# Kernel optimization log

Hardware: AMD Instinct MI355X
Metric: run time of the kernel (lower is better)

Reference implementation:

```python
import jax, jax.numpy as jnp
import numpy as np

B, T, H = 4, 1024, 4096
N_Q, N_KV, HD = 32, 8, 128
N_REP = N_Q // N_KV
THETA = 10000.0


def setup_inputs() -> dict:
    key = jax.random.key(0)
    k0, k1, k2 = jax.random.split(key, 3)
    x = jax.random.normal(k0, (B, T, H), dtype=jnp.float32)
    w_qkv = jax.random.normal(k1, ((N_Q + 2 * N_KV) * HD, H), dtype=jnp.float32) * 0.02
    w_proj = jax.random.normal(k2, (N_Q * HD, H), dtype=jnp.float32).T * 0.02  # [H, N_Q*HD] -> stored as [out,in]=[4096,4096]
    # real RoPE frequencies, matching precompute_freqs_cis(theta=10000)
    inv_freq = 1.0 / (THETA ** (np.arange(0, HD, 2, dtype=np.float32) / HD))  # [HD/2]
    angles = np.arange(T, dtype=np.float32)[:, None] * inv_freq[None, :]      # [T, HD/2]
    freqs_cos = jnp.asarray(np.cos(angles))
    freqs_sin = jnp.asarray(np.sin(angles))
    return {"x": x, "w_qkv": w_qkv, "w_proj": w_proj,
            "freqs_cos": freqs_cos, "freqs_sin": freqs_sin}


def _rope(x, cos, sin):
    # x: [B, T, nH, HD]; consecutive pairs (x[2i], x[2i+1]) form complex numbers
    x0 = x[..., 0::2]
    x1 = x[..., 1::2]
    c = cos[None, :, None, :]
    s = sin[None, :, None, :]
    r0 = x0 * c - x1 * s
    r1 = x0 * s + x1 * c
    return jnp.stack([r0, r1], axis=-1).reshape(x.shape)


def reference(x, w_qkv, w_proj, freqs_cos, freqs_sin):
    q_per_kv = N_Q // N_KV
    qkv = jnp.einsum('bth,oh->bto', x, w_qkv)                 # [B,T,(N_Q+2*N_KV)*HD]
    qkv = qkv.reshape(B, T, N_KV, q_per_kv + 2, HD)           # interleaved GQA layout
    q = qkv[:, :, :, :q_per_kv, :].reshape(B, T, N_Q, HD)
    k = qkv[:, :, :, q_per_kv, :]                              # [B,T,N_KV,HD]
    v = qkv[:, :, :, q_per_kv + 1, :]
    q = _rope(q, freqs_cos, freqs_sin)
    k = _rope(k, freqs_cos, freqs_sin)
    k = jnp.repeat(k, N_REP, axis=2)                           # [B,T,N_Q,HD]
    v = jnp.repeat(v, N_REP, axis=2)
    q = q.transpose(0, 2, 1, 3)                                # [B,H,T,HD]
    k = k.transpose(0, 2, 1, 3)
    v = v.transpose(0, 2, 1, 3)
    scale = 1.0 / jnp.sqrt(jnp.float32(HD))
    scores = jnp.einsum('bhqd,bhkd->bhqk', q, k) * scale       # [B,H,T,T]
    causal = jnp.tril(jnp.ones((T, T), dtype=bool))
    scores = jnp.where(causal[None, None], scores, jnp.finfo(scores.dtype).min)
    attn = jax.nn.softmax(scores, axis=-1)
    out = jnp.einsum('bhqk,bhkd->bhqd', attn, v)               # [B,H,T,HD]
    out = out.transpose(0, 2, 1, 3).reshape(B, T, N_Q * HD)
    return jnp.einsum('bto,ho->bth', out, w_proj)              # RowParallel proj, [B,T,H]
```

## Files before the change

kernel.cpp:

```cpp
#include <hip/hip_runtime.h>
#include <cstddef>

#define DEVINL __device__ __forceinline__

typedef float f32x4 __attribute__((ext_vector_type(4)));
typedef __bf16 bf16x8 __attribute__((ext_vector_type(8)));

DEVINL unsigned short f2bf(float f) {
  union { float f; unsigned int u; } v; v.f = f;
  unsigned int u = v.u;
  unsigned int r = (u + 0x7fffu + ((u >> 16) & 1u)) >> 16;
  return (unsigned short)r;
}
DEVINL float bf2f(unsigned short s) {
  union { unsigned int u; float f; } v; v.u = ((unsigned int)s) << 16;
  return v.f;
}
DEVINL uint4 pack8(const unsigned short o[8]) {
  uint4 r;
  r.x = (unsigned int)o[0] | ((unsigned int)o[1] << 16);
  r.y = (unsigned int)o[2] | ((unsigned int)o[3] << 16);
  r.z = (unsigned int)o[4] | ((unsigned int)o[5] << 16);
  r.w = (unsigned int)o[6] | ((unsigned int)o[7] << 16);
  return r;
}
DEVINL void gload16(const void* g, void* l) {
  __builtin_amdgcn_global_load_lds(
      (__attribute__((address_space(1))) void*)g,
      (__attribute__((address_space(3))) void*)l, 16, 0, 0);
}

__global__ __launch_bounds__(256) void k_cvt(const float* __restrict__ in,
                                             unsigned short* __restrict__ out, int n4) {
  int i = blockIdx.x * 256 + threadIdx.x;
  if (i >= n4) return;
  float4 v = ((const float4*)in)[i];
  ushort4 o;
  o.x = f2bf(v.x); o.y = f2bf(v.y); o.z = f2bf(v.z); o.w = f2bf(v.w);
  ((ushort4*)out)[i] = o;
}

template <int OUT_BF16>
__global__ __launch_bounds__(512, 1) void k_gemm256(const unsigned short* __restrict__ A,
                                                    const unsigned short* __restrict__ Bt,
                                                    void* __restrict__ Cout,
                                                    int M, int N, int K) {
  __shared__ __align__(16) unsigned short As[2][2][256 * 32];
  __shared__ __align__(16) unsigned short Bs[2][2][256 * 32];
  const int t = threadIdx.x, lane = t & 63;
  const int wid = t >> 6, wm = wid >> 2, wn = wid & 3;
  const int fr = lane & 15, kq = lane >> 4;
  const int nwg = gridDim.x * gridDim.y;
  int lin = blockIdx.y * gridDim.x + blockIdx.x;
  lin = (lin & 7) * (nwg >> 3) + (lin >> 3);
  const int bx = lin % gridDim.x, by = lin / gridDim.x;
  const int row0 = by * 256, col0 = bx * 256;
  const int NT = K >> 6;

  int srow[2], sgs[2];
#pragma unroll
  for (int i = 0; i < 2; ++i) {
    const int off = (i * 512 + t) * 16;
    srow[i] = off >> 6;
    sgs[i] = (((off >> 4) & 3) - (srow[i] >> 1)) & 3;
  }

#define STAGE_A(KT, KS)                                                        \
  do {                                                                         \
    const int b_ = (KT) & 1;                                                   \
    _Pragma("unroll") for (int i = 0; i < 2; ++i)                              \
        gload16(A + (size_t)(row0 + srow[i]) * K + (KT) * 64 + (KS) * 32 +     \
                    sgs[i] * 8,                                                \
                (char*)&As[b_][KS][0] + i * 8192 + wid * 1024);                \
  } while (0)
#define STAGE_B(KT, KS)                                                        \
  do {                                                                         \
    const int b_ = (KT) & 1;                                                   \
    _Pragma("unroll") for (int i = 0; i < 2; ++i)                              \
        gload16(Bt + (size_t)(col0 + srow[i]) * K + (KT) * 64 + (KS) * 32 +    \
                    sgs[i] * 8,                                                \
                (char*)&Bs[b_][KS][0] + i * 8192 + wid * 1024);                \
  } while (0)
#define LDFRAG(BUFP, ROW) \
  (*(const bf16x8*)((const char*)(BUFP) + (ROW) * 64 + ((((ROW) >> 1) + kq & 3) << 4)))

  f32x4 acc[8][4];
#pragma unroll
  for (int m = 0; m < 8; ++m)
#pragma unroll
    for (int n = 0; n < 4; ++n) acc[m][n] = f32x4{0.f, 0.f, 0.f, 0.f};

  STAGE_A(0, 0); STAGE_B(0, 0); STAGE_A(0, 1); STAGE_B(0, 1);
  STAGE_A(1, 0); STAGE_B(1, 0);
  asm volatile("s_waitcnt vmcnt(4)" ::: "memory");
  __builtin_amdgcn_s_barrier();

  for (int kt = 0; kt < NT; ++kt) {
    const unsigned short* As0 = &As[kt & 1][0][0];
    const unsigned short* As1 = &As[kt & 1][1][0];
    const unsigned short* Bs0 = &Bs[kt & 1][0][0];
    const unsigned short* Bs1 = &Bs[kt & 1][1][0];
    bf16x8 a0[4], a1[4], b0[4], b1[4];

#pragma unroll
    for (int m = 0; m < 4; ++m) a0[m] = LDFRAG(As0, wm * 128 + m * 16 + fr);
#pragma unroll
    for (int n = 0; n < 4; ++n) b0[n] = LDFRAG(Bs0, wn * 64 + n * 16 + fr);
    if (kt + 1 < NT) STAGE_A(kt + 1, 1);
    __builtin_amdgcn_sched_barrier(0);
    __builtin_amdgcn_s_barrier();
    asm volatile("s_waitcnt lgkmcnt(0)" ::: "memory");
    __builtin_amdgcn_sched_barrier(0);
    __builtin_amdgcn_s_setprio(1);
#pragma unroll
    for (int m = 0; m < 4; ++m)
#pragma unroll
      for (int n = 0; n < 4; ++n)
        acc[m][n] = __builtin_amdgcn_mfma_f32_16x16x32_bf16(a0[m], b0[n], acc[m][n], 0, 0, 0);
    __builtin_amdgcn_s_setprio(0);
    __builtin_amdgcn_s_barrier();

#pragma unroll
    for (int m = 0; m < 4; ++m) a1[m] = LDFRAG(As0, wm * 128 + 64 + m * 16 + fr);
    if (kt + 1 < NT) STAGE_B(kt + 1, 1);
    __builtin_amdgcn_sched_barrier(0);
    __builtin_amdgcn_s_barrier();
    asm volatile("s_waitcnt lgkmcnt(0)" ::: "memory");
    __builtin_amdgcn_sched_barrier(0);
    __builtin_amdgcn_s_setprio(1);
#pragma unroll
    for (int m = 0; m < 4; ++m)
#pragma unroll
      for (int n = 0; n < 4; ++n)
        acc[m + 4][n] = __builtin_amdgcn_mfma_f32_16x16x32_bf16(a1[m], b0[n], acc[m + 4][n], 0, 0, 0);
    __builtin_amdgcn_s_setprio(0);
    __builtin_amdgcn_s_barrier();

#pragma unroll
    for (int m = 0; m < 4; ++m) a0[m] = LDFRAG(As1, wm * 128 + m * 16 + fr);
#pragma unroll
    for (int n = 0; n < 4; ++n) b1[n] = LDFRAG(Bs1, wn * 64 + n * 16 + fr);
    if (kt + 2 < NT) STAGE_A(kt + 2, 0);
    __builtin_amdgcn_sched_barrier(0);
    __builtin_amdgcn_s_barrier();
    asm volatile("s_waitcnt lgkmcnt(0)" ::: "memory");
    __builtin_amdgcn_sched_barrier(0);
    __builtin_amdgcn_s_setprio(1);
#pragma unroll
    for (int m = 0; m < 4; ++m)
#pragma unroll
      for (int n = 0; n < 4; ++n)
        acc[m][n] = __builtin_amdgcn_mfma_f32_16x16x32_bf16(a0[m], b1[n], acc[m][n], 0, 0, 0);
    __builtin_amdgcn_s_setprio(0);
    __builtin_amdgcn_s_barrier();

#pragma unroll
    for (int m = 0; m < 4; ++m) a1[m] = LDFRAG(As1, wm * 128 + 64 + m * 16 + fr);
    if (kt + 1 < NT) {
      if (kt + 2 < NT) asm volatile("s_waitcnt vmcnt(2)" ::: "memory");
      else             asm volatile("s_waitcnt vmcnt(0)" ::: "memory");
    }
    if (kt + 2 < NT) STAGE_B(kt + 2, 0);
    __builtin_amdgcn_sched_barrier(0);
    __builtin_amdgcn_s_barrier();
    asm volatile("s_waitcnt lgkmcnt(0)" ::: "memory");
    __builtin_amdgcn_sched_barrier(0);
    __builtin_amdgcn_s_setprio(1);
#pragma unroll
    for (int m = 0; m < 4; ++m)
#pragma unroll
      for (int n = 0; n < 4; ++n)
        acc[m + 4][n] = __builtin_amdgcn_mfma_f32_16x16x32_bf16(a1[m], b1[n], acc[m + 4][n], 0, 0, 0);
    __builtin_amdgcn_s_setprio(0);
    __builtin_amdgcn_s_barrier();
  }
#undef STAGE_A
#undef STAGE_B
#undef LDFRAG

  const int rsub = kq * 4;
#pragma unroll
  for (int m = 0; m < 8; ++m)
#pragma unroll
    for (int n = 0; n < 4; ++n)
#pragma unroll
      for (int r = 0; r < 4; ++r) {
        const size_t row = (size_t)row0 + wm * 128 + m * 16 + rsub + r;
        const size_t col = (size_t)col0 + wn * 64 + n * 16 + fr;
        if (OUT_BF16)
          ((unsigned short*)Cout)[row * N + col] = f2bf(acc[m][n][r]);
        else
          ((float*)Cout)[row * N + col] = acc[m][n][r];
      }
}

__global__ __launch_bounds__(256) void k_rope(const unsigned short* __restrict__ qkv,
                                              const float* __restrict__ fcos,
                                              const float* __restrict__ fsin,
                                              unsigned short* __restrict__ Qb,
                                              unsigned short* __restrict__ Kb) {
  const int idx = blockIdx.x * 256 + threadIdx.x;
  if (idx >= 4096 * 640) return;
  const int bt = idx / 640;
  const int r = idx - bt * 640;
  const int g = r / 80;
  const int rr = r - g * 80;
  const int slot = rr >> 4;
  const int d0 = (rr & 15) * 8;
  const int o0 = g * 768 + slot * 128 + d0;
  const int b = bt >> 10, tt = bt & 1023;

  uint4 raw = *(const uint4*)&qkv[(size_t)bt * 6144 + o0];
  unsigned short us[8] = {
      (unsigned short)(raw.x & 0xffff), (unsigned short)(raw.x >> 16),
      (unsigned short)(raw.y & 0xffff), (unsigned short)(raw.y >> 16),
      (unsigned short)(raw.z & 0xffff), (unsigned short)(raw.z >> 16),
      (unsigned short)(raw.w & 0xffff), (unsigned short)(raw.w >> 16)};

  float4 c = *(const float4*)&fcos[tt * 64 + (d0 >> 1)];
  float4 s = *(const float4*)&fsin[tt * 64 + (d0 >> 1)];
  const float sc = (slot < 4) ? 0.08838834764831845f : 1.0f;
  float cj[4] = {c.x, c.y, c.z, c.w};
  float sj[4] = {s.x, s.y, s.z, s.w};
  unsigned short os[8];
#pragma unroll
  for (int j = 0; j < 4; ++j) {
    float x0 = bf2f(us[2 * j]), x1 = bf2f(us[2 * j + 1]);
    os[2 * j] = f2bf((x0 * cj[j] - x1 * sj[j]) * sc);
    os[2 * j + 1] = f2bf((x0 * sj[j] + x1 * cj[j]) * sc);
  }
  if (slot < 4) {
    const int h = g * 4 + slot;
    *(uint4*)&Qb[((size_t)(b * 32 + h) * 1024 + tt) * 128 + d0] = pack8(os);
  } else {
    *(uint4*)&Kb[((size_t)(b * 8 + g) * 1024 + tt) * 128 + d0] = pack8(os);
  }
}

__global__ __launch_bounds__(256) void k_vtrans(const unsigned short* __restrict__ qkv,
                                                unsigned short* __restrict__ VT) {
  const int t = threadIdx.x;
  const int tt0 = blockIdx.x * 128;
  const int bg = blockIdx.y;
  const int b = bg >> 3, g = bg & 7;
  const int tj = t & 15;
  const int ti = t >> 4;
  union U4 { uint4 v; unsigned int u[4]; };
  U4 in[8], out[8];
  const unsigned short* src =
      qkv + (size_t)(b * 1024 + tt0 + ti * 8) * 6144 + g * 768 + 640 + tj * 8;
#pragma unroll
  for (int r = 0; r < 8; ++r) in[r].v = *(const uint4*)(src + (size_t)r * 6144);
#pragma unroll
  for (int c = 0; c < 8; ++c) {
    const unsigned int sel = (c & 1) ? 0x07060302u : 0x05040100u;
    const int dw = c >> 1;
#pragma unroll
    for (int w = 0; w < 4; ++w)
      out[c].u[w] = __builtin_amdgcn_perm(in[2 * w + 1].u[dw], in[2 * w].u[dw], sel);
  }
  unsigned short* dst = VT + (size_t)bg * 131072 + (size_t)(tj * 8) * 1024 + tt0 + ti * 8;
#pragma unroll
  for (int c = 0; c < 8; ++c) *(uint4*)(dst + (size_t)c * 1024) = out[c].v;
}

__global__ __launch_bounds__(256) void k_attn(const unsigned short* __restrict__ Qb,
                                              const unsigned short* __restrict__ Kb,
                                              const unsigned short* __restrict__ VT,
                                              unsigned short* __restrict__ AO) {
  __shared__ __align__(16) unsigned short Ks[64 * 128];
  __shared__ __align__(16) unsigned short Vt[128 * 64];
  __shared__ __align__(16) unsigned short Ps[4 * 16 * 64];
  const int t = threadIdx.x, lane = t & 63, wv = t >> 6;
  const int bh = blockIdx.y;
  const int b = bh >> 5, h = bh & 31, g = h >> 2;
  const int qi = 15 - blockIdx.x;
  const int q0 = qi * 64;
  const int fr = lane & 15, kq = lane >> 4;
  const size_t kvbase = (size_t)(b * 8 + g) * (1024 * 128);
  const size_t vtbase = (size_t)(b * 8 + g) * (128 * 1024);

  bf16x8 qf[4];
  {
    const unsigned short* Qp = Qb + ((size_t)(b * 32 + h) * 1024 + q0 + wv * 16 + fr) * 128;
#pragma unroll
    for (int ks = 0; ks < 4; ++ks) qf[ks] = *(const bf16x8*)&Qp[ks * 32 + kq * 8];
  }
  float mrow[4] = {-1e30f, -1e30f, -1e30f, -1e30f};
  float lrow[4] = {0.f, 0.f, 0.f, 0.f};
  f32x4 of[8];
#pragma unroll
  for (int n = 0; n < 8; ++n) of[n] = f32x4{0.f, 0.f, 0.f, 0.f};

  for (int kt = 0; kt <= qi; ++kt) {
    const int kv0 = kt * 64;
#pragma unroll
    for (int it = 0; it < 4; ++it) {
      const int off = it * 4096 + wv * 1024 + lane * 16;
      {
        const int r = off >> 8, cb = off & 255;
        const int scb = cb ^ ((r & 7) << 4);
        gload16(Kb + kvbase + (size_t)(kv0 + r) * 128 + (scb >> 1),
                (char*)Ks + it * 4096 + wv * 1024);
      }
      {
        const int rd = off >> 7, cb = off & 127;
        const int scb = cb ^ ((rd & 7) << 4);
        gload16(VT + vtbase + (size_t)rd * 1024 + kv0 + (scb >> 1),
                (char*)Vt + it * 4096 + wv * 1024);
      }
    }
    __syncthreads();

    f32x4 sacc[4];
#pragma unroll
    for (int n = 0; n < 4; ++n) sacc[n] = f32x4{0.f, 0.f, 0.f, 0.f};
#pragma unroll
    for (int n = 0; n < 4; ++n) {
      const int row = n * 16 + fr;
      const int sw = (row & 7) << 4;
#pragma unroll
      for (int ks = 0; ks < 4; ++ks) {
        bf16x8 kf = *(const bf16x8*)((const char*)Ks + row * 256 + ((ks * 64 + kq * 16) ^ sw));
        sacc[n] = __builtin_amdgcn_mfma_f32_16x16x32_bf16(qf[ks], kf, sacc[n], 0, 0, 0);
      }
    }

#pragma unroll
    for (int rg = 0; rg < 4; ++rg) {
      const int qrow = q0 + wv * 16 + kq * 4 + rg;
      float s[4];
#pragma unroll
      for (int n = 0; n < 4; ++n) {
        s[n] = sacc[n][rg];
        if (kv0 + n * 16 + fr > qrow) s[n] = -1e30f;
      }
      float mx = fmaxf(fmaxf(s[0], s[1]), fmaxf(s[2], s[3]));
#pragma unroll
      for (int o = 1; o < 16; o <<= 1) mx = fmaxf(mx, __shfl_xor(mx, o));
      const float mnew = fmaxf(mrow[rg], mx);
      float p[4];
#pragma unroll
      for (int n = 0; n < 4; ++n) p[n] = __expf(s[n] - mnew);
      float sum = (p[0] + p[1]) + (p[2] + p[3]);
#pragma unroll
      for (int o = 1; o < 16; o <<= 1) sum += __shfl_xor(sum, o);
      const float fac = __expf(mrow[rg] - mnew);
      lrow[rg] = lrow[rg] * fac + sum;
      mrow[rg] = mnew;
#pragma unroll
      for (int n = 0; n < 8; ++n) of[n][rg] *= fac;
      const int q = kq * 4 + rg;
      const int swp = (q & 7) << 4;
#pragma unroll
      for (int n = 0; n < 4; ++n)
        *(unsigned short*)((char*)Ps + wv * 2048 + q * 128 + ((2 * (n * 16 + fr)) ^ swp)) =
            f2bf(p[n]);
    }
    asm volatile("s_waitcnt lgkmcnt(0)" ::: "memory");
    __builtin_amdgcn_sched_barrier(0);

    bf16x8 pa[2];
#pragma unroll
    for (int kk = 0; kk < 2; ++kk)
      pa[kk] = *(const bf16x8*)((const char*)Ps + wv * 2048 + fr * 128 +
                                ((kk * 64 + kq * 16) ^ ((fr & 7) << 4)));
#pragma unroll
    for (int n = 0; n < 8; ++n) {
      const int row = n * 16 + fr;
      const int sw = (row & 7) << 4;
#pragma unroll
      for (int kk = 0; kk < 2; ++kk) {
        bf16x8 vf = *(const bf16x8*)((const char*)Vt + row * 128 + ((kk * 64 + kq * 16) ^ sw));
        of[n] = __builtin_amdgcn_mfma_f32_16x16x32_bf16(pa[kk], vf, of[n], 0, 0, 0);
      }
    }
    __syncthreads();
  }

  float inv[4];
#pragma unroll
  for (int rg = 0; rg < 4; ++rg) inv[rg] = 1.0f / lrow[rg];
#pragma unroll
  for (int n = 0; n < 8; ++n)
#pragma unroll
    for (int rg = 0; rg < 4; ++rg) {
      const size_t row = (size_t)b * 1024 + q0 + wv * 16 + kq * 4 + rg;
      const size_t col = (size_t)h * 128 + n * 16 + fr;
      AO[row * 4096 + col] = f2bf(of[n][rg] * inv[rg]);
    }
}

extern "C" void kernel_launch(void* const* d_in, const int* in_sizes, int n_in,
                              void* d_out, int out_size, void* d_ws, size_t ws_size,
                              hipStream_t stream) {
  const float* x = (const float*)d_in[0];
  const float* w_qkv = (const float*)d_in[1];
  const float* w_proj = (const float*)d_in[2];
  const float* fcos = (const float*)d_in[3];
  const float* fsin = (const float*)d_in[4];
  float* out = (float*)d_out;

  char* ws = (char*)d_ws;
  unsigned short* XB    = (unsigned short*)(ws + 0);
  unsigned short* WQKVB = (unsigned short*)(ws + 33554432);
  unsigned short* QKVB  = (unsigned short*)(ws + 83886080);
  unsigned short* QB    = (unsigned short*)(ws + 134217728);
  unsigned short* KB    = (unsigned short*)(ws + 167772160);
  unsigned short* VTB   = (unsigned short*)(ws + 176160768);
  unsigned short* WPROJB = XB;
  unsigned short* AOB    = QKVB;

  k_cvt<<<16384, 256, 0, stream>>>(x, XB, 4194304);
  k_cvt<<<24576, 256, 0, stream>>>(w_qkv, WQKVB, 6291456);
  k_gemm256<1><<<dim3(24, 16), 512, 0, stream>>>(XB, WQKVB, QKVB, 4096, 6144, 4096);
  k_cvt<<<16384, 256, 0, stream>>>(w_proj, WPROJB, 4194304);
  k_rope<<<10240, 256, 0, stream>>>(QKVB, fcos, fsin, QB, KB);
  k_vtrans<<<dim3(8, 32), 256, 0, stream>>>(QKVB, VTB);
  k_attn<<<dim3(16, 128), 256, 0, stream>>>(QB, KB, VTB, AOB);
  k_gemm256<0><<<dim3(16, 16), 512, 0, stream>>>(AOB, WPROJB, out, 4096, 4096, 4096);
}
```

Measured before the change: 596.4 us.

## Share KV tiles across GQA heads in attention with double-buffered loads

The attention kernel now launches one 512-thread block per (batch, KV group, query tile). Its eight waves cover the four query heads that share a KV head, with 32 query rows each. K/V tiles are loaded once per group rather than once per head, and are double-buffered so the next tile's global loads overlap the current tile's compute. In the GEMM, the vmcnt waits move to allow more outstanding loads before each barrier. In exchange, registers and LDS per block go up and there are fewer, larger blocks, which may lower occupancy.

```diff
diff --git a/kernel.cpp b/kernel.cpp
--- a/kernel.cpp
+++ b/kernel.cpp
@@ -92,7 +92,7 @@
 
   STAGE_A(0, 0); STAGE_B(0, 0); STAGE_A(0, 1); STAGE_B(0, 1);
   STAGE_A(1, 0); STAGE_B(1, 0);
-  asm volatile("s_waitcnt vmcnt(4)" ::: "memory");
+  asm volatile("s_waitcnt vmcnt(8)" ::: "memory");
   __builtin_amdgcn_s_barrier();
 
   for (int kt = 0; kt < NT; ++kt) {
@@ -134,6 +134,9 @@
       for (int n = 0; n < 4; ++n)
         acc[m + 4][n] = __builtin_amdgcn_mfma_f32_16x16x32_bf16(a1[m], b0[n], acc[m + 4][n], 0, 0, 0);
     __builtin_amdgcn_s_setprio(0);
+    if (kt + 1 < NT) asm volatile("s_waitcnt vmcnt(8)" ::: "memory");
+    else             asm volatile("s_waitcnt vmcnt(0)" ::: "memory");
+    __builtin_amdgcn_sched_barrier(0);
     __builtin_amdgcn_s_barrier();
 
 #pragma unroll
@@ -156,10 +159,6 @@
 
 #pragma unroll
     for (int m = 0; m < 4; ++m) a1[m] = LDFRAG(As1, wm * 128 + 64 + m * 16 + fr);
-    if (kt + 1 < NT) {
-      if (kt + 2 < NT) asm volatile("s_waitcnt vmcnt(2)" ::: "memory");
-      else             asm volatile("s_waitcnt vmcnt(0)" ::: "memory");
-    }
     if (kt + 2 < NT) STAGE_B(kt + 2, 0);
     __builtin_amdgcn_sched_barrier(0);
     __builtin_amdgcn_s_barrier();
@@ -172,6 +171,9 @@
       for (int n = 0; n < 4; ++n)
         acc[m + 4][n] = __builtin_amdgcn_mfma_f32_16x16x32_bf16(a1[m], b1[n], acc[m + 4][n], 0, 0, 0);
     __builtin_amdgcn_s_setprio(0);
+    if (kt + 2 < NT)      asm volatile("s_waitcnt vmcnt(8)" ::: "memory");
+    else if (kt + 1 < NT) asm volatile("s_waitcnt vmcnt(4)" ::: "memory");
+    __builtin_amdgcn_sched_barrier(0);
     __builtin_amdgcn_s_barrier();
   }
 #undef STAGE_A
@@ -264,131 +266,183 @@
   for (int c = 0; c < 8; ++c) *(uint4*)(dst + (size_t)c * 1024) = out[c].v;
 }
 
-__global__ __launch_bounds__(256) void k_attn(const unsigned short* __restrict__ Qb,
-                                              const unsigned short* __restrict__ Kb,
-                                              const unsigned short* __restrict__ VT,
-                                              unsigned short* __restrict__ AO) {
-  __shared__ __align__(16) unsigned short Ks[64 * 128];
-  __shared__ __align__(16) unsigned short Vt[128 * 64];
-  __shared__ __align__(16) unsigned short Ps[4 * 16 * 64];
-  const int t = threadIdx.x, lane = t & 63, wv = t >> 6;
-  const int bh = blockIdx.y;
-  const int b = bh >> 5, h = bh & 31, g = h >> 2;
-  const int qi = 15 - blockIdx.x;
+__global__ __launch_bounds__(512, 1) void k_attn(const unsigned short* __restrict__ Qb,
+                                                 const unsigned short* __restrict__ Kb,
+                                                 const unsigned short* __restrict__ VT,
+                                                 unsigned short* __restrict__ AO) {
+  __shared__ __align__(16) unsigned short Ks[2][64 * 128];
+  __shared__ __align__(16) unsigned short Vt[2][128 * 64];
+  __shared__ __align__(16) unsigned short Ps[8][32 * 64];
+  const int t = threadIdx.x, lane = t & 63, wid = t >> 6;
+  const int hh = wid >> 1, qh = wid & 1;
+  const int bg = blockIdx.x, b = bg >> 3, g = bg & 7;
+  const int qi = 15 - (int)blockIdx.y;
   const int q0 = qi * 64;
+  const int h = g * 4 + hh;
   const int fr = lane & 15, kq = lane >> 4;
-  const size_t kvbase = (size_t)(b * 8 + g) * (1024 * 128);
-  const size_t vtbase = (size_t)(b * 8 + g) * (128 * 1024);
-
-  bf16x8 qf[4];
+  const size_t kvbase = (size_t)bg * (1024 * 128);
+  const size_t vtbase = (size_t)bg * (128 * 1024);
+
+#define ASTAGE(TILE, BUF)                                                      \
+  do {                                                                         \
+    const int kv0_ = (TILE) * 64;                                              \
+    _Pragma("unroll") for (int it = 0; it < 2; ++it) {                         \
+      const int off = it * 8192 + t * 16;                                      \
+      const int r_ = off >> 8, cb_ = off & 255;                                \
+      const int scb_ = cb_ ^ ((r_ & 7) << 4);                                  \
+      gload16(Kb + kvbase + (size_t)(kv0_ + r_) * 128 + (scb_ >> 1),           \
+              (char*)Ks[BUF] + off);                                           \
+    }                                                                          \
+    _Pragma("unroll") for (int it = 0; it < 2; ++it) {                         \
+      const int off = it * 8192 + t * 16;                                      \
+      const int rd_ = off >> 7, cb_ = off & 127;                               \
+      const int scb_ = cb_ ^ ((rd_ & 7) << 4);                                 \
+      gload16(VT + vtbase + (size_t)rd_ * 1024 + kv0_ + (scb_ >> 1),           \
+              (char*)Vt[BUF] + off);                                           \
+    }                                                                          \
+  } while (0)
+
+  bf16x8 qf[2][4];
   {
-    const unsigned short* Qp = Qb + ((size_t)(b * 32 + h) * 1024 + q0 + wv * 16 + fr) * 128;
-#pragma unroll
-    for (int ks = 0; ks < 4; ++ks) qf[ks] = *(const bf16x8*)&Qp[ks * 32 + kq * 8];
-  }
-  float mrow[4] = {-1e30f, -1e30f, -1e30f, -1e30f};
-  float lrow[4] = {0.f, 0.f, 0.f, 0.f};
-  f32x4 of[8];
-#pragma unroll
-  for (int n = 0; n < 8; ++n) of[n] = f32x4{0.f, 0.f, 0.f, 0.f};
-
-  for (int kt = 0; kt <= qi; ++kt) {
+    const unsigned short* Qp0 = Qb + ((size_t)(b * 32 + h) * 1024 + q0 + qh * 32) * 128;
+#pragma unroll
+    for (int qr = 0; qr < 2; ++qr)
+#pragma unroll
+      for (int ks = 0; ks < 4; ++ks)
+        qf[qr][ks] = *(const bf16x8*)&Qp0[(size_t)(qr * 16 + fr) * 128 + ks * 32 + kq * 8];
+  }
+  float mrow[2][4], lrow[2][4];
+#pragma unroll
+  for (int qr = 0; qr < 2; ++qr)
+#pragma unroll
+    for (int rg = 0; rg < 4; ++rg) { mrow[qr][rg] = -1e30f; lrow[qr][rg] = 0.f; }
+  f32x4 of[2][8];
+#pragma unroll
+  for (int qr = 0; qr < 2; ++qr)
+#pragma unroll
+    for (int n = 0; n < 8; ++n) of[qr][n] = f32x4{0.f, 0.f, 0.f, 0.f};
+
+  const int ntiles = qi + 1;
+  ASTAGE(0, 0);
+
+  for (int kt = 0; kt < ntiles; ++kt) {
+    const int buf = kt & 1;
     const int kv0 = kt * 64;
-#pragma unroll
-    for (int it = 0; it < 4; ++it) {
-      const int off = it * 4096 + wv * 1024 + lane * 16;
-      {
-        const int r = off >> 8, cb = off & 255;
-        const int scb = cb ^ ((r & 7) << 4);
-        gload16(Kb + kvbase + (size_t)(kv0 + r) * 128 + (scb >> 1),
-                (char*)Ks + it * 4096 + wv * 1024);
-      }
-      {
-        const int rd = off >> 7, cb = off & 127;
-        const int scb = cb ^ ((rd & 7) << 4);
-        gload16(VT + vtbase + (size_t)rd * 1024 + kv0 + (scb >> 1),
-                (char*)Vt + it * 4096 + wv * 1024);
-      }
+    if (kt + 1 < ntiles) {
+      ASTAGE(kt + 1, buf ^ 1);
+      asm volatile("s_waitcnt vmcnt(4)" ::: "memory");
+    } else {
+      asm volatile("s_waitcnt vmcnt(0)" ::: "memory");
     }
-    __syncthreads();
-
-    f32x4 sacc[4];
-#pragma unroll
-    for (int n = 0; n < 4; ++n) sacc[n] = f32x4{0.f, 0.f, 0.f, 0.f};
+    __builtin_amdgcn_s_barrier();
+    __builtin_amdgcn_sched_barrier(0);
+
+    f32x4 sacc[2][4];
+#pragma unroll
+    for (int qr = 0; qr < 2; ++qr)
+#pragma unroll
+      for (int n = 0; n < 4; ++n) sacc[qr][n] = f32x4{0.f, 0.f, 0.f, 0.f};
 #pragma unroll
     for (int n = 0; n < 4; ++n) {
       const int row = n * 16 + fr;
       const int sw = (row & 7) << 4;
-#pragma unroll
-      for (int ks = 0; ks < 4; ++ks) {
-        bf16x8 kf = *(const bf16x8*)((const char*)Ks + row * 256 + ((ks * 64 + kq * 16) ^ sw));
-        sacc[n] = __builtin_amdgcn_mfma_f32_16x16x32_bf16(qf[ks], kf, sacc[n], 0, 0, 0);
+      bf16x8 kf[4];
+#pragma unroll
+      for (int ks = 0; ks < 4; ++ks)
+        kf[ks] = *(const bf16x8*)((const char*)Ks[buf] + row * 256 + ((ks * 64 + kq * 16) ^ sw));
+      __builtin_amdgcn_s_setprio(1);
+#pragma unroll
+      for (int qr = 0; qr < 2; ++qr)
+#pragma unroll
+        for (int ks = 0; ks < 4; ++ks)
+          sacc[qr][n] =
+              __builtin_amdgcn_mfma_f32_16x16x32_bf16(qf[qr][ks], kf[ks], sacc[qr][n], 0, 0, 0);
+      __builtin_amdgcn_s_setprio(0);
+    }
+
+#pragma unroll
+    for (int qr = 0; qr < 2; ++qr)
+#pragma unroll
+      for (int rg = 0; rg < 4; ++rg) {
+        const int qrow = q0 + qh * 32 + qr * 16 + kq * 4 + rg;
+        float s[4];
+#pragma unroll
+        for (int n = 0; n < 4; ++n) {
+          s[n] = sacc[qr][n][rg];
+          if (kv0 + n * 16 + fr > qrow) s[n] = -1e30f;
+        }
+        float mx = fmaxf(fmaxf(s[0], s[1]), fmaxf(s[2], s[3]));
+#pragma unroll
+        for (int o = 1; o < 16; o <<= 1) mx = fmaxf(mx, __shfl_xor(mx, o));
+        const float mnew = fmaxf(mrow[qr][rg], mx);
+        float p[4];
+#pragma unroll
+        for (int n = 0; n < 4; ++n) p[n] = __expf(s[n] - mnew);
+        float sum = (p[0] + p[1]) + (p[2] + p[3]);
+#pragma unroll
+        for (int o = 1; o < 16; o <<= 1) sum += __shfl_xor(sum, o);
+        const float fac = __expf(mrow[qr][rg] - mnew);
+        lrow[qr][rg] = lrow[qr][rg] * fac + sum;
+        mrow[qr][rg] = mnew;
+#pragma unroll
+        for (int n = 0; n < 8; ++n) of[qr][n][rg] *= fac;
+        const int q = qr * 16 + kq * 4 + rg;
+        const int swp = (q & 7) << 4;
+#pragma unroll
+        for (int n = 0; n < 4; ++n)
+          *(unsigned short*)((char*)Ps[wid] + q * 128 + ((2 * (n * 16 + fr)) ^ swp)) =
+              f2bf(p[n]);
       }
+    asm volatile("s_waitcnt lgkmcnt(0)" ::: "memory");
+    __builtin_amdgcn_sched_barrier(0);
+
+    bf16x8 pa[2][2];
+#pragma unroll
+    for (int qr = 0; qr < 2; ++qr) {
+      const int prow = qr * 16 + fr;
+      const int swp = (prow & 7) << 4;
+#pragma unroll
+      for (int kk = 0; kk < 2; ++kk)
+        pa[qr][kk] = *(const bf16x8*)((const char*)Ps[wid] + prow * 128 +
+                                      ((kk * 64 + kq * 16) ^ swp));
     }
-
-#pragma unroll
-    for (int rg = 0; rg < 4; ++rg) {
-      const int qrow = q0 + wv * 16 + kq * 4 + rg;
-      float s[4];
-#pragma unroll
-      for (int n = 0; n < 4; ++n) {
-        s[n] = sacc[n][rg];
-        if (kv0 + n * 16 + fr > qrow) s[n] = -1e30f;
-      }
-      float mx = fmaxf(fmaxf(s[0], s[1]), fmaxf(s[2], s[3]));
-#pragma unroll
-      for (int o = 1; o < 16; o <<= 1) mx = fmaxf(mx, __shfl_xor(mx, o));
-      const float mnew = fmaxf(mrow[rg], mx);
-      float p[4];
-#pragma unroll
-      for (int n = 0; n < 4; ++n) p[n] = __expf(s[n] - mnew);
-      float sum = (p[0] + p[1]) + (p[2] + p[3]);
-#pragma unroll
-      for (int o = 1; o < 16; o <<= 1) sum += __shfl_xor(sum, o);
-      const float fac = __expf(mrow[rg] - mnew);
-      lrow[rg] = lrow[rg] * fac + sum;
-      mrow[rg] = mnew;
-#pragma unroll
-      for (int n = 0; n < 8; ++n) of[n][rg] *= fac;
-      const int q = kq * 4 + rg;
-      const int swp = (q & 7) << 4;
-#pragma unroll
-      for (int n = 0; n < 4; ++n)
-        *(unsigned short*)((char*)Ps + wv * 2048 + q * 128 + ((2 * (n * 16 + fr)) ^ swp)) =
-            f2bf(p[n]);
-    }
-    asm volatile("s_waitcnt lgkmcnt(0)" ::: "memory");
-    __builtin_amdgcn_sched_barrier(0);
-
-    bf16x8 pa[2];
-#pragma unroll
-    for (int kk = 0; kk < 2; ++kk)
-      pa[kk] = *(const bf16x8*)((const char*)Ps + wv * 2048 + fr * 128 +
-                                ((kk * 64 + kq * 16) ^ ((fr & 7) << 4)));
 #pragma unroll
     for (int n = 0; n < 8; ++n) {
       const int row = n * 16 + fr;
       const int sw = (row & 7) << 4;
-#pragma unroll
-      for (int kk = 0; kk < 2; ++kk) {
-        bf16x8 vf = *(const bf16x8*)((const char*)Vt + row * 128 + ((kk * 64 + kq * 16) ^ sw));
-        of[n] = __builtin_amdgcn_mfma_f32_16x16x32_bf16(pa[kk], vf, of[n], 0, 0, 0);
+      bf16x8 vf[2];
+#pragma unroll
+      for (int kk = 0; kk < 2; ++kk)
+        vf[kk] = *(const bf16x8*)((const char*)Vt[buf] + row * 128 + ((kk * 64 + kq * 16) ^ sw));
+      __builtin_amdgcn_s_setprio(1);
+#pragma unroll
+      for (int qr = 0; qr < 2; ++qr)
+#pragma unroll
+        for (int kk = 0; kk < 2; ++kk)
+          of[qr][n] = __builtin_amdgcn_mfma_f32_16x16x32_bf16(pa[qr][kk], vf[kk], of[qr][n], 0, 0, 0);
+      __builtin_amdgcn_s_setprio(0);
+    }
+    asm volatile("s_waitcnt lgkmcnt(0)" ::: "memory");
+    __builtin_amdgcn_sched_barrier(0);
+    __builtin_amdgcn_s_barrier();
+  }
+#undef ASTAGE
+
+  float inv[2][4];
+#pragma unroll
+  for (int qr = 0; qr < 2; ++qr)
+#pragma unroll
+    for (int rg = 0; rg < 4; ++rg) inv[qr][rg] = 1.0f / lrow[qr][rg];
+#pragma unroll
+  for (int qr = 0; qr < 2; ++qr)
+#pragma unroll
+    for (int n = 0; n < 8; ++n)
+#pragma unroll
+      for (int rg = 0; rg < 4; ++rg) {
+        const size_t row = (size_t)b * 1024 + q0 + qh * 32 + qr * 16 + kq * 4 + rg;
+        const size_t col = (size_t)h * 128 + n * 16 + fr;
+        AO[row * 4096 + col] = f2bf(of[qr][n][rg] * inv[qr][rg]);
       }
-    }
-    __syncthreads();
-  }
-
-  float inv[4];
-#pragma unroll
-  for (int rg = 0; rg < 4; ++rg) inv[rg] = 1.0f / lrow[rg];
-#pragma unroll
-  for (int n = 0; n < 8; ++n)
-#pragma unroll
-    for (int rg = 0; rg < 4; ++rg) {
-      const size_t row = (size_t)b * 1024 + q0 + wv * 16 + kq * 4 + rg;
-      const size_t col = (size_t)h * 128 + n * 16 + fr;
-      AO[row * 4096 + col] = f2bf(of[n][rg] * inv[rg]);
-    }
 }
 
 extern "C" void kernel_launch(void* const* d_in, const int* in_sizes, int n_in,
@@ -417,6 +471,6 @@
   k_cvt<<<16384, 256, 0, stream>>>(w_proj, WPROJB, 4194304);
   k_rope<<<10240, 256, 0, stream>>>(QKVB, fcos, fsin, QB, KB);
   k_vtrans<<<dim3(8, 32), 256, 0, stream>>>(QKVB, VTB);
-  k_attn<<<dim3(16, 128), 256, 0, stream>>>(QB, KB, VTB, AOB);
+  k_attn<<<dim3(32, 16), 512, 0, stream>>>(QB, KB, VTB, AOB);
   k_gemm256<0><<<dim3(16, 16), 512, 0, stream>>>(AOB, WPROJB, out, 4096, 4096, 4096);
 }
```

Result: faster. 512.3 us (-14.1%).
